# Kernel optimization log

Measured on AMD Instinct MI355X. Metric: run time of the kernel, lower is better.

Reference implementation:

```python
import jax, jax.numpy as jnp
import numpy as np

MUL = 64            # channel multiplicity per l
B = 8               # number of systems (equal-size MOLE segments)
N = 64000           # total edges
E = 8               # experts
OFFS = (0, 1, 4)    # per-l offsets inside D_total=9 rotation matrix
DTOT = 9
DIM = MUL * DTOT    # 1152

# ---- z-rotation scatter pattern (build_z_rot_multi): diag=cos(f*ang), antidiag=sin(f*ang), f = l - i ----
_rows, _anti, _freq = [], [], []
for l, off in zip(range(3), OFFS):
    for i in range(2 * l + 1):
        _rows.append(off + i); _anti.append(off + 2 * l - i); _freq.append(l - i)
_rows = np.array(_rows); _anti = np.array(_anti)
ROWS = jnp.array(_rows); FREQ = jnp.array(np.array(_freq, dtype=np.float32))
_nc = _rows != _anti  # exclude diag/antidiag overlap (center) from sin scatter
ROWS_NC = jnp.array(_rows[_nc]); ANTI_NC = jnp.array(_anti[_nc]); NCJ = jnp.array(np.where(_nc)[0])

# ---- per-m gather/scatter index tables (m_in_mask/m_out_mask) for irreps 64x0e+64x1o+64x2e ----
_c = np.arange(MUL)
M0_IDX = jnp.array(np.concatenate([_c, 64 + 3 * _c + 1, 256 + 5 * _c + 2]))                 # [192] centers
M1_IDX = jnp.array(np.stack([np.concatenate([64 + 3 * _c, 256 + 5 * _c + 1]),
                             np.concatenate([64 + 3 * _c + 2, 256 + 5 * _c + 3])], 1))      # [128,2] (-m,+m)
M2_IDX = jnp.array(np.stack([256 + 5 * _c, 256 + 5 * _c + 4], 1))                            # [64,2]


def _z_rot(angles):
    # scatter cos/sin into dense [N,9,9] block-diagonal z-rotation (irregular-access hot spot)
    c = jnp.cos(angles[:, None] * FREQ[None, :])
    s = jnp.sin(angles[:, None] * FREQ[None, :])
    X = jnp.zeros((angles.shape[0], DTOT, DTOT), angles.dtype)
    X = X.at[:, ROWS, ROWS].set(c)
    X = X.at[:, ROWS_NC, ANTI_NC].set(s[:, NCJ])
    return X


def _wigner(alpha, beta, gamma, Jf):
    Xa, Xb, Xc = _z_rot(alpha), _z_rot(beta), _z_rot(gamma)
    return Xa @ Jf @ Xb @ Jf @ Xc  # [N,9,9]


def _rotate(x, D):
    # apply block-diagonal Wigner D per l-block of each channel
    parts, col = [], 0
    for l, off in zip(range(3), OFFS):
        d = 2 * l + 1
        xl = x[:, col:col + MUL * d].reshape(-1, MUL, d)
        Dl = D[:, off:off + d, off:off + d]
        parts.append(jnp.einsum('nij,ncj->nci', Dl, xl).reshape(-1, MUL * d))
        col += MUL * d
    return jnp.concatenate(parts, axis=1)


def _mole(x, coef, We, Ws, be=None, bs=None):
    # MOLELinear: per-system expert-mixed weights + shared expert; equal-size segments
    W = jnp.einsum('be,eoi->boi', coef, We) + Ws[None]
    y = jnp.einsum('bti,boi->bto', x.reshape(B, -1, x.shape[-1]), W)
    if be is not None:
        y = y + (jnp.einsum('be,eo->bo', coef, be) + bs)[:, None, :]
    return y.reshape(x.shape[:-1] + (W.shape[1],))


def setup_inputs() -> dict:
    key = jax.random.key(0)
    ks = jax.random.split(key, 16)
    k0 = 1.0 / np.sqrt(192.0); k1 = 1.0 / np.sqrt(128.0 * 2.0); k2 = 1.0 / np.sqrt(64.0 * 2.0)
    two_pi = 6.2831853
    return dict(
        x=jax.random.normal(ks[0], (N, DIM), jnp.float32),
        alpha=jax.random.uniform(ks[1], (N,), jnp.float32, 0.0, two_pi),
        beta=jax.random.uniform(ks[2], (N,), jnp.float32, 0.0, two_pi),
        gamma=jax.random.uniform(ks[3], (N,), jnp.float32, 0.0, two_pi),
        coefficients=jax.nn.softmax(jax.random.normal(ks[4], (B, E), jnp.float32), axis=-1),
        Jd1=jax.random.normal(ks[5], (3, 3), jnp.float32),
        Jd2=jax.random.normal(ks[6], (5, 5), jnp.float32),
        w_m0=jax.random.normal(ks[7], (E, 192, 192), jnp.float32) * k0,
        b_m0=jax.random.normal(ks[8], (E, 192), jnp.float32) * k0,
        ws_m0=jax.random.normal(ks[9], (192, 192), jnp.float32) * k0,
        bs_m0=jax.random.normal(ks[10], (192,), jnp.float32) * k0,
        w_m1=jax.random.normal(ks[11], (E, 256, 128), jnp.float32) * k1,
        ws_m1=jax.random.normal(ks[12], (256, 128), jnp.float32) * k1,
        w_m2=jax.random.normal(ks[13], (E, 128, 64), jnp.float32) * k2,
        ws_m2=jax.random.normal(ks[14], (128, 64), jnp.float32) * k2,
    )


def reference(x, alpha, beta, gamma, coefficients, Jd1, Jd2,
              w_m0, b_m0, ws_m0, bs_m0, w_m1, ws_m1, w_m2, ws_m2):
    # block-diagonal J (Jd constants per l)
    Jf = (jnp.zeros((DTOT, DTOT), x.dtype)
          .at[0, 0].set(1.0)
          .at[1:4, 1:4].set(Jd1)
          .at[4:9, 4:9].set(Jd2))
    # rotate_in
    xr = _rotate(x, _wigner(alpha, beta, gamma, Jf))
    out = jnp.zeros((x.shape[0], DIM), x.dtype)
    # m = 0 path (MOLE linear with bias)
    out = out.at[:, M0_IDX].set(_mole(xr[:, M0_IDX], coefficients, w_m0, ws_m0, b_m0, bs_m0))
    # m > 0 paths (SO2_m_Linear, no bias)
    for IDX, We, Ws in ((M1_IDX, w_m1, ws_m1), (M2_IDX, w_m2, ws_m2)):
        C_out = We.shape[1] // 2
        xg = xr[:, IDX.reshape(-1)].reshape(-1, IDX.shape[0], 2).transpose(0, 2, 1)  # [N,2,C] rows=(-m,+m)
        y = _mole(xg, coefficients, We, Ws)                                            # [N,2,2*C_out]
        y_r, y_i = y[..., :C_out], y[..., C_out:]
        om = y_r[:, 0] - y_i[:, 1]
        op = y_r[:, 1] + y_i[:, 0]
        out = out.at[:, IDX.reshape(-1)].set(jnp.stack([om, op], -1).reshape(-1, 2 * C_out))
    # rotate_out (inverse rotation)
    out = _rotate(out, _wigner(-gamma, -beta, -alpha, Jf))
    return out
```

## Files before the change

kernel.cpp:

```cpp
#include <hip/hip_runtime.h>
#include <cstddef>

#define NS 64000
#define GROUP 8000
#define TM 32

typedef __bf16 bf16x8 __attribute__((ext_vector_type(8)));
typedef float floatx4 __attribute__((ext_vector_type(4)));
typedef unsigned short ushort_t;

static const size_t BY_W0 = 0;
static const size_t BY_W1 = BY_W0 + 589824;
static const size_t BY_W2 = BY_W1 + 1048576;
static const size_t BY_B0 = BY_W2 + 262144;

__device__ __forceinline__ unsigned short f2bf(float f) {
    unsigned u = __float_as_uint(f);
    u += 0x7fff + ((u >> 16) & 1);
    return (unsigned short)(u >> 16);
}

__global__ __launch_bounds__(256) void mix_kernel(
    const float* __restrict__ coef,
    const float* __restrict__ w_m0, const float* __restrict__ b_m0,
    const float* __restrict__ ws_m0, const float* __restrict__ bs_m0,
    const float* __restrict__ w_m1, const float* __restrict__ ws_m1,
    const float* __restrict__ w_m2, const float* __restrict__ ws_m2,
    ushort_t* __restrict__ W0, float* __restrict__ B0,
    ushort_t* __restrict__ W1, ushort_t* __restrict__ W2)
{
    int tid = blockIdx.x * 256 + threadIdx.x;
    if (tid < 294912) {
        int b = tid / 36864, rem = tid % 36864;
        float s = ws_m0[rem];
        #pragma unroll
        for (int e = 0; e < 8; e++) s += coef[b * 8 + e] * w_m0[e * 36864 + rem];
        W0[tid] = f2bf(s);
    } else if (tid < 296448) {
        int i2 = tid - 294912;
        int b = i2 / 192, o = i2 % 192;
        float s = bs_m0[o];
        #pragma unroll
        for (int e = 0; e < 8; e++) s += coef[b * 8 + e] * b_m0[e * 192 + o];
        B0[i2] = s;
    } else if (tid < 820736) {
        int i3 = tid - 296448;
        int b = i3 >> 16, rem = i3 & 65535;
        int o = rem >> 8, i = rem & 255;
        int r, cc; float sign = 1.0f;
        if (o < 128) { if (i < 128) { r = o;       cc = i; } else { r = 128 + o;      cc = i - 128; sign = -1.0f; } }
        else { int o2 = o - 128; if (i < 128) { r = 128 + o2; cc = i; } else { r = o2; cc = i - 128; } }
        int idx = r * 128 + cc;
        float s = ws_m1[idx];
        #pragma unroll
        for (int e = 0; e < 8; e++) s += coef[b * 8 + e] * w_m1[e * 32768 + idx];
        W1[i3] = f2bf(sign * s);
    } else if (tid < 951808) {
        int i4 = tid - 820736;
        int b = i4 >> 14, rem = i4 & 16383;
        int o = rem >> 7, i = rem & 127;
        int r, cc; float sign = 1.0f;
        if (o < 64) { if (i < 64) { r = o;      cc = i; } else { r = 64 + o;      cc = i - 64; sign = -1.0f; } }
        else { int o2 = o - 64; if (i < 64) { r = 64 + o2; cc = i; } else { r = o2; cc = i - 64; } }
        int idx = r * 64 + cc;
        float s = ws_m2[idx];
        #pragma unroll
        for (int e = 0; e < 8; e++) s += coef[b * 8 + e] * w_m2[e * 8192 + idx];
        W2[i4] = f2bf(sign * s);
    }
}

__device__ __forceinline__ void zrot1(float& v0, float& v2, float c, float s) {
    float t0 = c * v0 + s * v2;
    v2 = -s * v0 + c * v2;
    v0 = t0;
}
__device__ __forceinline__ void j1mul(const float* J, float& v0, float& v1, float& v2) {
    float w0 = J[0] * v0 + J[1] * v1 + J[2] * v2;
    float w1 = J[3] * v0 + J[4] * v1 + J[5] * v2;
    float w2 = J[6] * v0 + J[7] * v1 + J[8] * v2;
    v0 = w0; v1 = w1; v2 = w2;
}
__device__ __forceinline__ void zrot2(float& u0, float& u1, float& u3, float& u4,
                                      float c1, float s1, float c2, float s2) {
    float t0 = c2 * u0 + s2 * u4;
    u4 = -s2 * u0 + c2 * u4;
    u0 = t0;
    float t1 = c1 * u1 + s1 * u3;
    u3 = -s1 * u1 + c1 * u3;
    u1 = t1;
}
__device__ __forceinline__ void j2mul(const float* J, float& u0, float& u1, float& u2, float& u3, float& u4) {
    float w0 = J[0]  * u0 + J[1]  * u1 + J[2]  * u2 + J[3]  * u3 + J[4]  * u4;
    float w1 = J[5]  * u0 + J[6]  * u1 + J[7]  * u2 + J[8]  * u3 + J[9]  * u4;
    float w2 = J[10] * u0 + J[11] * u1 + J[12] * u2 + J[13] * u3 + J[14] * u4;
    float w3 = J[15] * u0 + J[16] * u1 + J[17] * u2 + J[18] * u3 + J[19] * u4;
    float w4 = J[20] * u0 + J[21] * u1 + J[22] * u2 + J[23] * u3 + J[24] * u4;
    u0 = w0; u1 = w1; u2 = w2; u3 = w3; u4 = w4;
}

__device__ __forceinline__ int sidx(int row, int k, int K) {
    int gr = (k >> 3) ^ (row & 7);
    return row * K + gr * 8 + (k & 7);
}
__device__ __forceinline__ float yread(const ushort_t* L, int row, int k, int K) {
    unsigned u = L[sidx(row, k, K)];
    return __uint_as_float(u << 16);
}

__device__ __forceinline__ void load_row(const float* __restrict__ x, int n, int c, float* v) {
    const float* xr = x + (size_t)n * 576;
    v[0] = xr[c];
    v[1] = xr[64 + 3 * c];  v[2] = xr[64 + 3 * c + 1];  v[3] = xr[64 + 3 * c + 2];
    v[4] = xr[256 + 5 * c]; v[5] = xr[256 + 5 * c + 1]; v[6] = xr[256 + 5 * c + 2];
    v[7] = xr[256 + 5 * c + 3]; v[8] = xr[256 + 5 * c + 4];
}

template<int K, int NT>
__device__ __forceinline__ void gemm_seg(
    floatx4 (*acc)[2],
    const ushort_t* __restrict__ Wseg,
    const ushort_t* XL_,
    int mi, int quad)
{
    #pragma unroll
    for (int k0 = 0; k0 < K; k0 += 32) {
        bf16x8 af[2];
        #pragma unroll
        for (int ms = 0; ms < 2; ms++) {
            int row = ms * 16 + mi;
            int gr = ((k0 >> 3) + quad) ^ (row & 7);
            af[ms] = *(const bf16x8*)&XL_[row * K + gr * 8];
        }
        #pragma unroll
        for (int t = 0; t < NT; t++) {
            bf16x8 bt = *(const bf16x8*)&Wseg[(size_t)(t * 16 + mi) * K + k0 + quad * 8];
            acc[t][0] = __builtin_amdgcn_mfma_f32_16x16x32_bf16(af[0], bt, acc[t][0], 0, 0, 0);
            acc[t][1] = __builtin_amdgcn_mfma_f32_16x16x32_bf16(af[1], bt, acc[t][1], 0, 0, 0);
        }
    }
}

template<int K, int NT, bool BIAS>
__device__ __forceinline__ void ywrite(
    floatx4 (*acc)[2], ushort_t* L, int n0, const float* __restrict__ bias,
    int mi, int quad)
{
    #pragma unroll
    for (int t = 0; t < NT; t++) {
        int col = n0 + t * 16 + mi;
        float bv = BIAS ? bias[col] : 0.f;
        int gc = col >> 3, kw = col & 7;
        #pragma unroll
        for (int ms = 0; ms < 2; ms++) {
            #pragma unroll
            for (int r = 0; r < 4; r++) {
                int m = ms * 16 + quad * 4 + r;
                L[m * K + ((gc ^ (m & 7)) * 8) + kw] = f2bf(acc[t][ms][r] + bv);
            }
        }
    }
}

__global__ __launch_bounds__(256, 2) void fused_kernel(
    const float* __restrict__ x,
    const float* __restrict__ alpha, const float* __restrict__ beta, const float* __restrict__ gamma_,
    const float* __restrict__ Jd1, const float* __restrict__ Jd2,
    const ushort_t* __restrict__ W0, const ushort_t* __restrict__ W1, const ushort_t* __restrict__ W2,
    const float* __restrict__ B0,
    float* __restrict__ out)
{
    __shared__ ushort_t XL[18432];
    __shared__ float TR[32 * 6];
    __shared__ float JL[34];

    ushort_t* X0L = XL;
    ushort_t* X1L = XL + 6144;
    ushort_t* X2L = XL + 14336;

    int t = threadIdx.x;
    int w = t >> 6, lane = t & 63;
    int g = blockIdx.x / 250;
    int base = g * GROUP + (blockIdx.x % 250) * TM;

    if (t < 32) {
        int n = base + t;
        float sa, ca, sb, cb, sg, cg;
        __sincosf(alpha[n],  &sa, &ca);
        __sincosf(beta[n],   &sb, &cb);
        __sincosf(gamma_[n], &sg, &cg);
        TR[t * 6 + 0] = sa; TR[t * 6 + 1] = ca;
        TR[t * 6 + 2] = sb; TR[t * 6 + 3] = cb;
        TR[t * 6 + 4] = sg; TR[t * 6 + 5] = cg;
    } else if (t < 66) {
        int j = t - 32;
        JL[j] = (j < 9) ? Jd1[j] : Jd2[j - 9];
    }
    __syncthreads();

    int c = lane;

    {
        float J1r[9], J2r[25];
        #pragma unroll
        for (int j = 0; j < 9; j++)  J1r[j] = JL[j];
        #pragma unroll
        for (int j = 0; j < 25; j++) J2r[j] = JL[9 + j];

        float va[9], vb[9];
        load_row(x, base + w * 8, c, va);
        #pragma unroll
        for (int i = 0; i < 8; i++) {
            float* cu = (i & 1) ? vb : va;
            float* nx = (i & 1) ? va : vb;
            if (i < 7) load_row(x, base + w * 8 + i + 1, c, nx);

            int nl = w * 8 + i;
            float sa = TR[nl * 6 + 0], ca = TR[nl * 6 + 1];
            float sb = TR[nl * 6 + 2], cb = TR[nl * 6 + 3];
            float sg = TR[nl * 6 + 4], cg = TR[nl * 6 + 5];
            float s2a = 2.f * sa * ca, c2a = ca * ca - sa * sa;
            float s2b = 2.f * sb * cb, c2b = cb * cb - sb * sb;
            float s2g = 2.f * sg * cg, c2g = cg * cg - sg * sg;

            float v0 = cu[1], v1 = cu[2], v2 = cu[3];
            zrot1(v0, v2, cg, sg);
            j1mul(J1r, v0, v1, v2);
            zrot1(v0, v2, cb, sb);
            j1mul(J1r, v0, v1, v2);
            zrot1(v0, v2, ca, sa);

            float u0 = cu[4], u1 = cu[5], u2 = cu[6], u3 = cu[7], u4 = cu[8];
            zrot2(u0, u1, u3, u4, cg, sg, c2g, s2g);
            j2mul(J2r, u0, u1, u2, u3, u4);
            zrot2(u0, u1, u3, u4, cb, sb, c2b, s2b);
            j2mul(J2r, u0, u1, u2, u3, u4);
            zrot2(u0, u1, u3, u4, ca, sa, c2a, s2a);

            X0L[sidx(nl, c, 192)]       = f2bf(cu[0]);
            X0L[sidx(nl, 64 + c, 192)]  = f2bf(v1);
            X0L[sidx(nl, 128 + c, 192)] = f2bf(u2);
            X1L[sidx(nl, c, 256)]       = f2bf(v0);
            X1L[sidx(nl, 64 + c, 256)]  = f2bf(u1);
            X1L[sidx(nl, 128 + c, 256)] = f2bf(v2);
            X1L[sidx(nl, 192 + c, 256)] = f2bf(u3);
            X2L[sidx(nl, c, 128)]       = f2bf(u0);
            X2L[sidx(nl, 64 + c, 128)]  = f2bf(u4);
        }
    }
    __syncthreads();

    int mi = lane & 15, quad = lane >> 4;
    int cg = w;
    floatx4 acc[10][2];
    #pragma unroll
    for (int a = 0; a < 10; a++)
        #pragma unroll
        for (int b2 = 0; b2 < 2; b2++) acc[a][b2] = (floatx4)0.f;

    const ushort_t* W0g = W0 + (size_t)g * 192 * 192;
    const ushort_t* W1g = W1 + (size_t)g * 256 * 256;
    const ushort_t* W2g = W2 + (size_t)g * 128 * 128;

    if (cg == 0) {
        gemm_seg<192, 10>(acc, W0g, X0L, mi, quad);
    } else if (cg == 1) {
        gemm_seg<256, 8>(acc, W1g, X1L, mi, quad);
    } else if (cg == 2) {
        gemm_seg<256, 8>(acc, W1g + (size_t)128 * 256, X1L, mi, quad);
    } else {
        gemm_seg<192, 2>(acc, W0g + (size_t)160 * 192, X0L, mi, quad);
        gemm_seg<128, 8>(acc + 2, W2g, X2L, mi, quad);
    }

    __syncthreads();

    const float* B0g = B0 + g * 192;
    if (cg == 0) {
        ywrite<192, 10, true>(acc, X0L, 0, B0g, mi, quad);
    } else if (cg == 1) {
        ywrite<256, 8, false>(acc, X1L, 0, nullptr, mi, quad);
    } else if (cg == 2) {
        ywrite<256, 8, false>(acc, X1L, 128, nullptr, mi, quad);
    } else {
        ywrite<192, 2, true>(acc, X0L, 160, B0g, mi, quad);
        ywrite<128, 8, false>(acc + 2, X2L, 0, nullptr, mi, quad);
    }
    __syncthreads();

    {
        float J1r[9], J2r[25];
        #pragma unroll
        for (int j = 0; j < 9; j++)  J1r[j] = JL[j];
        #pragma unroll
        for (int j = 0; j < 25; j++) J2r[j] = JL[9 + j];

        for (int i = 0; i < 8; i++) {
            int nl = w * 8 + i;
            float sa = -TR[nl * 6 + 0], ca = TR[nl * 6 + 1];
            float sb = -TR[nl * 6 + 2], cb = TR[nl * 6 + 3];
            float sg = -TR[nl * 6 + 4], cg = TR[nl * 6 + 5];
            float s2a = 2.f * sa * ca, c2a = ca * ca - sa * sa;
            float s2b = 2.f * sb * cb, c2b = cb * cb - sb * sb;
            float s2g = 2.f * sg * cg, c2g = cg * cg - sg * sg;

            float* orow = out + (size_t)(base + nl) * 576;

            orow[c] = yread(X0L, nl, c, 192);

            float v0 = yread(X1L, nl, c, 256);
            float v1 = yread(X0L, nl, 64 + c, 192);
            float v2 = yread(X1L, nl, 128 + c, 256);
            zrot1(v0, v2, ca, sa);
            j1mul(J1r, v0, v1, v2);
            zrot1(v0, v2, cb, sb);
            j1mul(J1r, v0, v1, v2);
            zrot1(v0, v2, cg, sg);
            orow[64 + 3 * c]     = v0;
            orow[64 + 3 * c + 1] = v1;
            orow[64 + 3 * c + 2] = v2;

            float u0 = yread(X2L, nl, c, 128);
            float u1 = yread(X1L, nl, 64 + c, 256);
            float u2 = yread(X0L, nl, 128 + c, 192);
            float u3 = yread(X1L, nl, 192 + c, 256);
            float u4 = yread(X2L, nl, 64 + c, 128);
            zrot2(u0, u1, u3, u4, ca, sa, c2a, s2a);
            j2mul(J2r, u0, u1, u2, u3, u4);
            zrot2(u0, u1, u3, u4, cb, sb, c2b, s2b);
            j2mul(J2r, u0, u1, u2, u3, u4);
            zrot2(u0, u1, u3, u4, cg, sg, c2g, s2g);
            orow[256 + 5 * c]     = u0;
            orow[256 + 5 * c + 1] = u1;
            orow[256 + 5 * c + 2] = u2;
            orow[256 + 5 * c + 3] = u3;
            orow[256 + 5 * c + 4] = u4;
        }
    }
}

extern "C" void kernel_launch(void* const* d_in, const int* in_sizes, int n_in,
                              void* d_out, int out_size, void* d_ws, size_t ws_size,
                              hipStream_t stream)
{
    const float* x      = (const float*)d_in[0];
    const float* alpha  = (const float*)d_in[1];
    const float* beta   = (const float*)d_in[2];
    const float* gamma_ = (const float*)d_in[3];
    const float* coef   = (const float*)d_in[4];
    const float* Jd1    = (const float*)d_in[5];
    const float* Jd2    = (const float*)d_in[6];
    const float* w_m0   = (const float*)d_in[7];
    const float* b_m0   = (const float*)d_in[8];
    const float* ws_m0  = (const float*)d_in[9];
    const float* bs_m0  = (const float*)d_in[10];
    const float* w_m1   = (const float*)d_in[11];
    const float* ws_m1  = (const float*)d_in[12];
    const float* w_m2   = (const float*)d_in[13];
    const float* ws_m2  = (const float*)d_in[14];

    char* wsb = (char*)d_ws;
    ushort_t* W0 = (ushort_t*)(wsb + BY_W0);
    ushort_t* W1 = (ushort_t*)(wsb + BY_W1);
    ushort_t* W2 = (ushort_t*)(wsb + BY_W2);
    float*    B0 = (float*)(wsb + BY_B0);
    float*    out = (float*)d_out;

    hipLaunchKernelGGL(mix_kernel, dim3(3718), dim3(256), 0, stream,
                       coef, w_m0, b_m0, ws_m0, bs_m0, w_m1, ws_m1, w_m2, ws_m2,
                       W0, B0, W1, W2);
    hipLaunchKernelGGL(fused_kernel, dim3(2000), dim3(256), 0, stream,
                       x, alpha, beta, gamma_, Jd1, Jd2, W0, W1, W2, B0, out);
}
```

Measured before the change: 351.7 us.

## Stage input and output rows through shared memory with coalesced 16-byte transfers

Adds a 36 KB fp32 shared staging buffer that holds 16 rows at a time. The input tile is loaded with fully coalesced float4 reads, issued ahead of the sincos setup, and the second half is prefetched into registers while the first is processed. Output is written to the buffer and then stored to global memory as contiguous float4s. This replaces strided per-lane scalar gathers and scatters (stride 3 and 5). The cost is more LDS, which may reduce the two-block occupancy target, plus extra barriers and 36 registers held for the prefetch.

```diff
diff --git a/kernel.cpp b/kernel.cpp
--- a/kernel.cpp
+++ b/kernel.cpp
@@ -108,14 +108,6 @@
     return __uint_as_float(u << 16);
 }
 
-__device__ __forceinline__ void load_row(const float* __restrict__ x, int n, int c, float* v) {
-    const float* xr = x + (size_t)n * 576;
-    v[0] = xr[c];
-    v[1] = xr[64 + 3 * c];  v[2] = xr[64 + 3 * c + 1];  v[3] = xr[64 + 3 * c + 2];
-    v[4] = xr[256 + 5 * c]; v[5] = xr[256 + 5 * c + 1]; v[6] = xr[256 + 5 * c + 2];
-    v[7] = xr[256 + 5 * c + 3]; v[8] = xr[256 + 5 * c + 4];
-}
-
 template<int K, int NT>
 __device__ __forceinline__ void gemm_seg(
     floatx4 (*acc)[2],
@@ -170,7 +162,8 @@
     const float* __restrict__ B0,
     float* __restrict__ out)
 {
-    __shared__ ushort_t XL[18432];
+    __shared__ __align__(16) ushort_t XL[18432];
+    __shared__ __align__(16) float SB[9216];
     __shared__ float TR[32 * 6];
     __shared__ float JL[34];
 
@@ -182,6 +175,15 @@
     int w = t >> 6, lane = t & 63;
     int g = blockIdx.x / 250;
     int base = g * GROUP + (blockIdx.x % 250) * TM;
+    int c = lane;
+
+    const float* xb = x + (size_t)base * 576;
+    float* ob = out + (size_t)base * 576;
+
+    floatx4 st0[9];
+    #pragma unroll
+    for (int r = 0; r < 9; r++)
+        st0[r] = *(const floatx4*)(xb + (r * 256 + t) * 4);
 
     if (t < 32) {
         int n = base + t;
@@ -196,9 +198,17 @@
         int j = t - 32;
         JL[j] = (j < 9) ? Jd1[j] : Jd2[j - 9];
     }
+
+    #pragma unroll
+    for (int r = 0; r < 9; r++)
+        *(floatx4*)&SB[(r * 256 + t) * 4] = st0[r];
+
+    floatx4 st1[9];
+    #pragma unroll
+    for (int r = 0; r < 9; r++)
+        st1[r] = *(const floatx4*)(xb + 9216 + (r * 256 + t) * 4);
+
     __syncthreads();
-
-    int c = lane;
 
     {
         float J1r[9], J2r[25];
@@ -207,45 +217,53 @@
         #pragma unroll
         for (int j = 0; j < 25; j++) J2r[j] = JL[9 + j];
 
-        float va[9], vb[9];
-        load_row(x, base + w * 8, c, va);
-        #pragma unroll
-        for (int i = 0; i < 8; i++) {
-            float* cu = (i & 1) ? vb : va;
-            float* nx = (i & 1) ? va : vb;
-            if (i < 7) load_row(x, base + w * 8 + i + 1, c, nx);
-
-            int nl = w * 8 + i;
-            float sa = TR[nl * 6 + 0], ca = TR[nl * 6 + 1];
-            float sb = TR[nl * 6 + 2], cb = TR[nl * 6 + 3];
-            float sg = TR[nl * 6 + 4], cg = TR[nl * 6 + 5];
-            float s2a = 2.f * sa * ca, c2a = ca * ca - sa * sa;
-            float s2b = 2.f * sb * cb, c2b = cb * cb - sb * sb;
-            float s2g = 2.f * sg * cg, c2g = cg * cg - sg * sg;
-
-            float v0 = cu[1], v1 = cu[2], v2 = cu[3];
-            zrot1(v0, v2, cg, sg);
-            j1mul(J1r, v0, v1, v2);
-            zrot1(v0, v2, cb, sb);
-            j1mul(J1r, v0, v1, v2);
-            zrot1(v0, v2, ca, sa);
-
-            float u0 = cu[4], u1 = cu[5], u2 = cu[6], u3 = cu[7], u4 = cu[8];
-            zrot2(u0, u1, u3, u4, cg, sg, c2g, s2g);
-            j2mul(J2r, u0, u1, u2, u3, u4);
-            zrot2(u0, u1, u3, u4, cb, sb, c2b, s2b);
-            j2mul(J2r, u0, u1, u2, u3, u4);
-            zrot2(u0, u1, u3, u4, ca, sa, c2a, s2a);
-
-            X0L[sidx(nl, c, 192)]       = f2bf(cu[0]);
-            X0L[sidx(nl, 64 + c, 192)]  = f2bf(v1);
-            X0L[sidx(nl, 128 + c, 192)] = f2bf(u2);
-            X1L[sidx(nl, c, 256)]       = f2bf(v0);
-            X1L[sidx(nl, 64 + c, 256)]  = f2bf(u1);
-            X1L[sidx(nl, 128 + c, 256)] = f2bf(v2);
-            X1L[sidx(nl, 192 + c, 256)] = f2bf(u3);
-            X2L[sidx(nl, c, 128)]       = f2bf(u0);
-            X2L[sidx(nl, 64 + c, 128)]  = f2bf(u4);
+        #pragma unroll
+        for (int ch = 0; ch < 2; ch++) {
+            #pragma unroll
+            for (int i = 0; i < 4; i++) {
+                int sr = w * 4 + i;
+                int nl = ch * 16 + sr;
+                const float* S = SB + sr * 576;
+                float sa = TR[nl * 6 + 0], ca = TR[nl * 6 + 1];
+                float sb = TR[nl * 6 + 2], cb = TR[nl * 6 + 3];
+                float sg = TR[nl * 6 + 4], cg = TR[nl * 6 + 5];
+                float s2a = 2.f * sa * ca, c2a = ca * ca - sa * sa;
+                float s2b = 2.f * sb * cb, c2b = cb * cb - sb * sb;
+                float s2g = 2.f * sg * cg, c2g = cg * cg - sg * sg;
+
+                float x0 = S[c];
+                float v0 = S[64 + 3 * c], v1 = S[64 + 3 * c + 1], v2 = S[64 + 3 * c + 2];
+                zrot1(v0, v2, cg, sg);
+                j1mul(J1r, v0, v1, v2);
+                zrot1(v0, v2, cb, sb);
+                j1mul(J1r, v0, v1, v2);
+                zrot1(v0, v2, ca, sa);
+
+                float u0 = S[256 + 5 * c], u1 = S[256 + 5 * c + 1], u2 = S[256 + 5 * c + 2],
+                      u3 = S[256 + 5 * c + 3], u4 = S[256 + 5 * c + 4];
+                zrot2(u0, u1, u3, u4, cg, sg, c2g, s2g);
+                j2mul(J2r, u0, u1, u2, u3, u4);
+                zrot2(u0, u1, u3, u4, cb, sb, c2b, s2b);
+                j2mul(J2r, u0, u1, u2, u3, u4);
+                zrot2(u0, u1, u3, u4, ca, sa, c2a, s2a);
+
+                X0L[sidx(nl, c, 192)]       = f2bf(x0);
+                X0L[sidx(nl, 64 + c, 192)]  = f2bf(v1);
+                X0L[sidx(nl, 128 + c, 192)] = f2bf(u2);
+                X1L[sidx(nl, c, 256)]       = f2bf(v0);
+                X1L[sidx(nl, 64 + c, 256)]  = f2bf(u1);
+                X1L[sidx(nl, 128 + c, 256)] = f2bf(v2);
+                X1L[sidx(nl, 192 + c, 256)] = f2bf(u3);
+                X2L[sidx(nl, c, 128)]       = f2bf(u0);
+                X2L[sidx(nl, 64 + c, 128)]  = f2bf(u4);
+            }
+            __syncthreads();
+            if (ch == 0) {
+                #pragma unroll
+                for (int r = 0; r < 9; r++)
+                    *(floatx4*)&SB[(r * 256 + t) * 4] = st1[r];
+                __syncthreads();
+            }
         }
     }
     __syncthreads();
@@ -295,46 +313,55 @@
         #pragma unroll
         for (int j = 0; j < 25; j++) J2r[j] = JL[9 + j];
 
-        for (int i = 0; i < 8; i++) {
-            int nl = w * 8 + i;
-            float sa = -TR[nl * 6 + 0], ca = TR[nl * 6 + 1];
-            float sb = -TR[nl * 6 + 2], cb = TR[nl * 6 + 3];
-            float sg = -TR[nl * 6 + 4], cg = TR[nl * 6 + 5];
-            float s2a = 2.f * sa * ca, c2a = ca * ca - sa * sa;
-            float s2b = 2.f * sb * cb, c2b = cb * cb - sb * sb;
-            float s2g = 2.f * sg * cg, c2g = cg * cg - sg * sg;
-
-            float* orow = out + (size_t)(base + nl) * 576;
-
-            orow[c] = yread(X0L, nl, c, 192);
-
-            float v0 = yread(X1L, nl, c, 256);
-            float v1 = yread(X0L, nl, 64 + c, 192);
-            float v2 = yread(X1L, nl, 128 + c, 256);
-            zrot1(v0, v2, ca, sa);
-            j1mul(J1r, v0, v1, v2);
-            zrot1(v0, v2, cb, sb);
-            j1mul(J1r, v0, v1, v2);
-            zrot1(v0, v2, cg, sg);
-            orow[64 + 3 * c]     = v0;
-            orow[64 + 3 * c + 1] = v1;
-            orow[64 + 3 * c + 2] = v2;
-
-            float u0 = yread(X2L, nl, c, 128);
-            float u1 = yread(X1L, nl, 64 + c, 256);
-            float u2 = yread(X0L, nl, 128 + c, 192);
-            float u3 = yread(X1L, nl, 192 + c, 256);
-            float u4 = yread(X2L, nl, 64 + c, 128);
-            zrot2(u0, u1, u3, u4, ca, sa, c2a, s2a);
-            j2mul(J2r, u0, u1, u2, u3, u4);
-            zrot2(u0, u1, u3, u4, cb, sb, c2b, s2b);
-            j2mul(J2r, u0, u1, u2, u3, u4);
-            zrot2(u0, u1, u3, u4, cg, sg, c2g, s2g);
-            orow[256 + 5 * c]     = u0;
-            orow[256 + 5 * c + 1] = u1;
-            orow[256 + 5 * c + 2] = u2;
-            orow[256 + 5 * c + 3] = u3;
-            orow[256 + 5 * c + 4] = u4;
+        #pragma unroll
+        for (int ch = 0; ch < 2; ch++) {
+            #pragma unroll
+            for (int i = 0; i < 4; i++) {
+                int sr = w * 4 + i;
+                int nl = ch * 16 + sr;
+                float* S = SB + sr * 576;
+                float sa = -TR[nl * 6 + 0], ca = TR[nl * 6 + 1];
+                float sb = -TR[nl * 6 + 2], cb = TR[nl * 6 + 3];
+                float sg = -TR[nl * 6 + 4], cg = TR[nl * 6 + 5];
+                float s2a = 2.f * sa * ca, c2a = ca * ca - sa * sa;
+                float s2b = 2.f * sb * cb, c2b = cb * cb - sb * sb;
+                float s2g = 2.f * sg * cg, c2g = cg * cg - sg * sg;
+
+                S[c] = yread(X0L, nl, c, 192);
+
+                float v0 = yread(X1L, nl, c, 256);
+                float v1 = yread(X0L, nl, 64 + c, 192);
+                float v2 = yread(X1L, nl, 128 + c, 256);
+                zrot1(v0, v2, ca, sa);
+                j1mul(J1r, v0, v1, v2);
+                zrot1(v0, v2, cb, sb);
+                j1mul(J1r, v0, v1, v2);
+                zrot1(v0, v2, cg, sg);
+                S[64 + 3 * c]     = v0;
+                S[64 + 3 * c + 1] = v1;
+                S[64 + 3 * c + 2] = v2;
+
+                float u0 = yread(X2L, nl, c, 128);
+                float u1 = yread(X1L, nl, 64 + c, 256);
+                float u2 = yread(X0L, nl, 128 + c, 192);
+                float u3 = yread(X1L, nl, 192 + c, 256);
+                float u4 = yread(X2L, nl, 64 + c, 128);
+                zrot2(u0, u1, u3, u4, ca, sa, c2a, s2a);
+                j2mul(J2r, u0, u1, u2, u3, u4);
+                zrot2(u0, u1, u3, u4, cb, sb, c2b, s2b);
+                j2mul(J2r, u0, u1, u2, u3, u4);
+                zrot2(u0, u1, u3, u4, cg, sg, c2g, s2g);
+                S[256 + 5 * c]     = u0;
+                S[256 + 5 * c + 1] = u1;
+                S[256 + 5 * c + 2] = u2;
+                S[256 + 5 * c + 3] = u3;
+                S[256 + 5 * c + 4] = u4;
+            }
+            __syncthreads();
+            #pragma unroll
+            for (int r = 0; r < 9; r++)
+                *(floatx4*)(ob + ch * 9216 + (r * 256 + t) * 4) = *(const floatx4*)&SB[(r * 256 + t) * 4];
+            if (ch == 0) __syncthreads();
         }
     }
 }
```

After: 349.3 us. Within noise of the previous version (-0.7%).
